# Performance work log

Measured on AMD Instinct MI355X. Metric: run time of the kernel, lower is better.

Reference implementation:

```python
import jax, jax.numpy as jnp
import numpy as np

D_MODEL = 1024
HEADS = 16
D_K = D_MODEL // HEADS
B, S = 2, 2048


def setup_inputs() -> dict:
    key = jax.random.key(0)
    ks = jax.random.split(key, 11)
    sc = 1.0 / np.sqrt(D_MODEL)
    inp = {
        "q": jax.random.normal(ks[0], (B, S, D_MODEL), jnp.float32),
        "k": jax.random.normal(ks[1], (B, S, D_MODEL), jnp.float32),
        "v": jax.random.normal(ks[2], (B, S, D_MODEL), jnp.float32),
        # causal mask, broadcastable to (B, H, S, S); 0 -> masked
        "mask": jnp.tril(jnp.ones((S, S), jnp.int32))[None, None],
        "w_q": jax.random.normal(ks[3], (D_MODEL, D_MODEL), jnp.float32) * sc,
        "b_q": jax.random.normal(ks[4], (D_MODEL,), jnp.float32) * sc,
        "w_k": jax.random.normal(ks[5], (D_MODEL, D_MODEL), jnp.float32) * sc,
        "b_k": jax.random.normal(ks[6], (D_MODEL,), jnp.float32) * sc,
        "w_v": jax.random.normal(ks[7], (D_MODEL, D_MODEL), jnp.float32) * sc,
        "b_v": jax.random.normal(ks[8], (D_MODEL,), jnp.float32) * sc,
        "w_o": jax.random.normal(ks[9], (D_MODEL, D_MODEL), jnp.float32) * sc,
        "b_o": jax.random.normal(ks[10], (D_MODEL,), jnp.float32) * sc,
    }
    return inp


def reference(q, k, v, mask, w_q, b_q, w_k, b_k, w_v, b_v, w_o, b_o):
    b = q.shape[0]
    # torch Linear: x @ W.T + b
    Q = q @ w_q.T + b_q
    K = k @ w_k.T + b_k
    V = v @ w_v.T + b_v
    # (B, S, D) -> (B, H, S, d_k)
    Q = Q.reshape(b, -1, HEADS, D_K).transpose(0, 2, 1, 3)
    K = K.reshape(b, -1, HEADS, D_K).transpose(0, 2, 1, 3)
    V = V.reshape(b, -1, HEADS, D_K).transpose(0, 2, 1, 3)
    scores = jnp.einsum("bhqd,bhkd->bhqk", Q, K) / np.sqrt(D_K).astype(np.float32)
    scores = jnp.where(mask == 0, -jnp.inf, scores)
    attn = jax.nn.softmax(scores, axis=-1)
    out = jnp.einsum("bhqk,bhkd->bhqd", attn, V)
    out = out.transpose(0, 2, 1, 3).reshape(b, -1, D_MODEL)
    # dropout is identity in eval mode
    return out @ w_o.T + b_o
```

## Files before the change

kernel.cpp:

```cpp
#include <hip/hip_runtime.h>
#include <math.h>

#define D_MODEL 1024
#define N_HEADS 16
#define DKH     64
#define BATCH   2
#define SEQ     2048
#define NT128   (SEQ/128)
#define PARTS_PER_BH 40

typedef unsigned short u16;
typedef __attribute__((ext_vector_type(8))) short short8;
typedef __attribute__((ext_vector_type(4))) float f32x4;

__device__ __forceinline__ u16 f2bf(float f) {
    unsigned u = __float_as_uint(f);
    u += 0x7fffu + ((u >> 16) & 1u);
    return (u16)(u >> 16);
}
__device__ __forceinline__ float bf2f(u16 x) {
    return __int_as_float(((int)x) << 16);
}

__device__ __forceinline__ void gll16(const void* g, void* l) {
    __builtin_amdgcn_global_load_lds((const __attribute__((address_space(1))) void*)g,
                                     (__attribute__((address_space(3))) void*)l, 16, 0, 0);
}

template<int CTRL>
__device__ __forceinline__ float rormax(float x) {
    int r = __builtin_amdgcn_update_dpp(__float_as_int(x), __float_as_int(x),
                                        CTRL, 0xf, 0xf, false);
    return fmaxf(x, __int_as_float(r));
}
__device__ __forceinline__ float rowmax16(float x) {
    x = rormax<0x121>(x);
    x = rormax<0x122>(x);
    x = rormax<0x124>(x);
    x = rormax<0x128>(x);
    return x;
}

__global__ __launch_bounds__(256)
void convert_kernel(const float* __restrict__ q, const float* __restrict__ k,
                    const float* __restrict__ v, const float* __restrict__ wq,
                    const float* __restrict__ wk, const float* __restrict__ wv,
                    const float* __restrict__ wo,
                    u16* __restrict__ qb, u16* __restrict__ kb, u16* __restrict__ vb,
                    u16* __restrict__ wqb, u16* __restrict__ wkb,
                    u16* __restrict__ wvb, u16* __restrict__ wob)
{
    const size_t NV = ((size_t)16 << 20) >> 3;
    for (size_t i = (size_t)blockIdx.x * blockDim.x + threadIdx.x; i < NV;
         i += (size_t)gridDim.x * blockDim.x) {
        const size_t e = i << 3;
        const float* s; u16* d; size_t off;
        if (e < ((size_t)12 << 20)) {
            const int seg = (int)(e >> 22);
            off = e & (((size_t)1 << 22) - 1);
            s = seg == 0 ? q : seg == 1 ? k : v;
            d = seg == 0 ? qb : seg == 1 ? kb : vb;
        } else {
            const size_t r = e - ((size_t)12 << 20);
            const int seg = (int)(r >> 20);
            off = r & (((size_t)1 << 20) - 1);
            s = seg == 0 ? wq : seg == 1 ? wk : seg == 2 ? wv : wo;
            d = seg == 0 ? wqb : seg == 1 ? wkb : seg == 2 ? wvb : wob;
        }
        const float4 f0 = *(const float4*)(s + off);
        const float4 f1 = *(const float4*)(s + off + 4);
        short8 o;
        o[0]=(short)f2bf(f0.x); o[1]=(short)f2bf(f0.y); o[2]=(short)f2bf(f0.z); o[3]=(short)f2bf(f0.w);
        o[4]=(short)f2bf(f1.x); o[5]=(short)f2bf(f1.y); o[6]=(short)f2bf(f1.z); o[7]=(short)f2bf(f1.w);
        *(short8*)(d + off) = o;
    }
}

#define GEMM_PREAMBLE                                                            \
    __shared__ __align__(16) u16 As[2][128][32];                                 \
    __shared__ __align__(16) u16 Bs[2][128][32];                                 \
    const int tid  = threadIdx.x;                                                \
    const int lane = tid & 63;                                                   \
    const int wid  = tid >> 6;                                                   \
    const int wm   = wid >> 1, wn = wid & 1;                                     \
    const int lr   = lane & 15, lg = lane >> 4;                                  \
    const int mb   = blockIdx.x * 128, nb = blockIdx.y * 128;                    \
    const int g_row = lane >> 2;                                                 \
    const int g_col = (lane & 3) << 3;                                           \
    const u16* Ab = A  + (size_t)mb * K;                                         \
    const u16* Bb = Bw + (size_t)nb * K;                                         \
    f32x4 acc[4][4];                                                             \
    _Pragma("unroll")                                                            \
    for (int i = 0; i < 4; ++i)                                                  \
        _Pragma("unroll")                                                        \
        for (int j = 0; j < 4; ++j) { f32x4 z = {0.f,0.f,0.f,0.f}; acc[i][j] = z; }

#define STAGE(buf, kt)                                                           \
    {                                                                            \
        _Pragma("unroll")                                                        \
        for (int t = 0; t < 2; ++t) {                                            \
            const int r0 = t*64 + wid*16;                                        \
            gll16(&Ab[(size_t)(r0 + g_row)*K + (kt) + g_col], &As[buf][r0][0]);  \
            gll16(&Bb[(size_t)(r0 + g_row)*K + (kt) + g_col], &Bs[buf][r0][0]);  \
        }                                                                        \
    }

#define GEMM_MAINLOOP                                                            \
    STAGE(0, 0)                                                                  \
    __syncthreads();                                                             \
    const int NK = K >> 5;                                                       \
    for (int it = 0; it < NK; ++it) {                                            \
        const int c = it & 1;                                                    \
        if (it + 1 < NK) STAGE(c ^ 1, (it + 1) << 5)                             \
        short8 a[4], b[4];                                                       \
        _Pragma("unroll")                                                        \
        for (int i = 0; i < 4; ++i) a[i] = *(const short8*)&As[c][wm*64 + i*16 + lr][lg*8]; \
        _Pragma("unroll")                                                        \
        for (int j = 0; j < 4; ++j) b[j] = *(const short8*)&Bs[c][wn*64 + j*16 + lr][lg*8]; \
        _Pragma("unroll")                                                        \
        for (int i = 0; i < 4; ++i)                                              \
            _Pragma("unroll")                                                    \
            for (int j = 0; j < 4; ++j)                                          \
                acc[i][j] = __builtin_amdgcn_mfma_f32_16x16x32_bf16(a[i], b[j], acc[i][j], 0, 0, 0); \
        __syncthreads();                                                         \
    }

__global__ __launch_bounds__(256, 3)
void gemm_qkv_kernel(const u16* __restrict__ qb, const u16* __restrict__ kb,
                     const u16* __restrict__ vb, const u16* __restrict__ wqb,
                     const u16* __restrict__ wkb, const u16* __restrict__ wvb,
                     const float* __restrict__ b_q, const float* __restrict__ b_k,
                     const float* __restrict__ b_v,
                     u16* __restrict__ Qh, u16* __restrict__ Kh, u16* __restrict__ Vt,
                     int M, int N, int K)
{
    const int z = blockIdx.z;
    const u16* A    = z == 0 ? qb  : z == 1 ? kb  : vb;
    const u16* Bw   = z == 0 ? wqb : z == 1 ? wkb : wvb;
    const float* bias = z == 0 ? b_q : z == 1 ? b_k : b_v;
    u16* dst        = z == 0 ? Qh  : z == 1 ? Kh  : Vt;
    const float scale = z == 0 ? 0.125f : 1.0f;

    GEMM_PREAMBLE
    GEMM_MAINLOOP

    #pragma unroll
    for (int i = 0; i < 4; ++i) {
        #pragma unroll
        for (int j = 0; j < 4; ++j) {
            const int mbase = mb + wm*64 + i*16 + lg*4;
            const int n     = nb + wn*64 + j*16 + lr;
            const float bn  = bias[n];
            const int h = n >> 6, d = n & 63;
            #pragma unroll
            for (int r = 0; r < 4; ++r) {
                const int m = mbase + r;
                const int b = m >> 11, s = m & (SEQ - 1);
                const float val = (acc[i][j][r] + bn) * scale;
                if (z == 2)
                    dst[(((size_t)(b*N_HEADS + h))*DKH + d)*SEQ + s] = f2bf(val);
                else
                    dst[(((size_t)(b*N_HEADS + h))*SEQ + s)*DKH + d] = f2bf(val);
            }
        }
    }
}

__global__ __launch_bounds__(256)
void gemm_out_kernel(const u16* __restrict__ A, const u16* __restrict__ Bw,
                     const float* __restrict__ bias, float* __restrict__ dst,
                     int M, int N, int K)
{
    GEMM_PREAMBLE
    GEMM_MAINLOOP

    #pragma unroll
    for (int i = 0; i < 4; ++i) {
        #pragma unroll
        for (int j = 0; j < 4; ++j) {
            const int mbase = mb + wm*64 + i*16 + lg*4;
            const int n     = nb + wn*64 + j*16 + lr;
            const float bn  = bias[n];
            #pragma unroll
            for (int r = 0; r < 4; ++r)
                dst[(size_t)(mbase + r) * N + n] = acc[i][j][r] + bn;
        }
    }
}

__device__ __forceinline__ void attn_step(
    const short8& aq0, const short8& aq1,
    f32x4 (&o)[4], f32x4& osum, float (&m_run)[4],
    const u16 (*__restrict__ Kl)[64], const u16 (*__restrict__ Vl)[64],
    u16 (*__restrict__ Pw)[72],
    int kvb, int qbw, int lr, int lg)
{
    const int ksw = (lr & 7) << 3;
    f32x4 s[4];
    #pragma unroll
    for (int cb = 0; cb < 4; ++cb) {
        const int kr = cb*16 + lr;
        f32x4 z = {0.f,0.f,0.f,0.f};
        short8 k0 = *(const short8*)&Kl[kr][( 0 + lg*8) ^ ksw];
        short8 k1 = *(const short8*)&Kl[kr][(32 + lg*8) ^ ksw];
        z = __builtin_amdgcn_mfma_f32_16x16x32_bf16(aq0, k0, z, 0, 0, 0);
        z = __builtin_amdgcn_mfma_f32_16x16x32_bf16(aq1, k1, z, 0, 0, 0);
        s[cb] = z;
    }

    if (kvb + 63 > qbw) {
        #pragma unroll
        for (int cb = 0; cb < 4; ++cb)
            #pragma unroll
            for (int r = 0; r < 4; ++r)
                if (kvb + cb*16 + lr > qbw + lg*4 + r) s[cb][r] = -INFINITY;
    }

    float tm[4];
    #pragma unroll
    for (int r = 0; r < 4; ++r)
        tm[r] = rowmax16(fmaxf(fmaxf(s[0][r], s[1][r]), fmaxf(s[2][r], s[3][r])));

    int need = 0;
    #pragma unroll
    for (int r = 0; r < 4; ++r) need |= (tm[r] > m_run[r] + 8.f) ? 1 : 0;
    if (__any(need)) {
        #pragma unroll
        for (int r = 0; r < 4; ++r) {
            const float mnew  = fmaxf(m_run[r], tm[r]);
            const float alpha = __expf(m_run[r] - mnew);
            m_run[r] = mnew;
            osum[r] *= alpha;
            #pragma unroll
            for (int db = 0; db < 4; ++db) o[db][r] *= alpha;
        }
    }
    #pragma unroll
    for (int r = 0; r < 4; ++r)
        #pragma unroll
        for (int cb = 0; cb < 4; ++cb)
            Pw[lg*4 + r][cb*16 + lr] = f2bf(__expf(s[cb][r] - m_run[r]));

    short8 vone;
    #pragma unroll
    for (int j = 0; j < 8; ++j) vone[j] = (short)0x3F80;
    #pragma unroll
    for (int ks = 0; ks < 2; ++ks) {
        short8 ap = *(short8*)&Pw[lr][ks*32 + lg*8];
        #pragma unroll
        for (int db = 0; db < 4; ++db) {
            const int vr = db*16 + lr;
            short8 bv = *(const short8*)&Vl[vr][(ks*32 + lg*8) ^ ksw];
            o[db] = __builtin_amdgcn_mfma_f32_16x16x32_bf16(ap, bv, o[db], 0, 0, 0);
        }
        osum = __builtin_amdgcn_mfma_f32_16x16x32_bf16(ap, vone, osum, 0, 0, 0);
    }
}

__global__ __launch_bounds__(512)
void flash_split_kernel(const u16* __restrict__ Qh, const u16* __restrict__ Kh,
                        const u16* __restrict__ Vt, u16* __restrict__ part_o,
                        float* __restrict__ part_ms)
{
    __shared__ __align__(16) u16 Kl[2][64][64];
    __shared__ __align__(16) u16 Vl[2][64][64];
    __shared__ __align__(16) u16 P[8][16][72];

    const int x = blockIdx.x;
    int t, ch;
    if      (x <  4) { t = x;                 ch = 0;        }
    else if (x < 12) { t = 4 + ((x-4) >> 1);  ch = (x-4)&1;  }
    else if (x < 24) { t = 8 + (x-12)/3;      ch = (x-12)%3; }
    else             { t = 12 + ((x-24) >> 2); ch = (x-24)&3; }

    const int tid  = threadIdx.x;
    const int lane = tid & 63;
    const int wid  = tid >> 6;
    const int lr   = lane & 15, lg = lane >> 4;
    const int bh   = blockIdx.y;
    const int qbw  = t*128 + wid*16;
    const size_t base = (size_t)bh * SEQ * DKH;

    const int c0      = ch * 8;
    const int nc_here = min(8, 2*(t+1) - c0);

    const int srow = tid >> 3;
    const int se0  = (tid & 7) << 3;
    const int sec  = se0 ^ ((srow & 7) << 3);

    short8 aq0 = *(const short8*)&Qh[base + (size_t)(qbw + lr)*DKH +  0 + lg*8];
    short8 aq1 = *(const short8*)&Qh[base + (size_t)(qbw + lr)*DKH + 32 + lg*8];

    f32x4 o[4], osum;
    float m_run[4];
    #pragma unroll
    for (int r = 0; r < 4; ++r) m_run[r] = -INFINITY;
    {
        f32x4 z = {0.f,0.f,0.f,0.f};
        osum = z;
        #pragma unroll
        for (int db = 0; db < 4; ++db) o[db] = z;
    }

    {
        const int kb0 = c0 * 64;
        short8 k0 = *(const short8*)&Kh[base + (size_t)(kb0 + srow)*DKH + se0];
        short8 v0 = *(const short8*)&Vt[base + (size_t)srow*SEQ + kb0 + se0];
        *(short8*)&Kl[0][srow][sec] = k0;
        *(short8*)&Vl[0][srow][sec] = v0;
    }
    __syncthreads();

    int cur = 0;
    for (int ci = 0; ci < nc_here; ++ci) {
        const int kvb = (c0 + ci) * 64;
        short8 nk0, nv0;
        const bool pref = (ci + 1 < nc_here);
        if (pref) {
            const int nb_ = kvb + 64;
            nk0 = *(const short8*)&Kh[base + (size_t)(nb_ + srow)*DKH + se0];
            nv0 = *(const short8*)&Vt[base + (size_t)srow*SEQ + nb_ + se0];
        }

        if (kvb <= qbw + 15)
            attn_step(aq0, aq1, o, osum, m_run, Kl[cur], Vl[cur], P[wid], kvb, qbw, lr, lg);

        __syncthreads();
        if (pref) {
            *(short8*)&Kl[cur^1][srow][sec] = nk0;
            *(short8*)&Vl[cur^1][srow][sec] = nv0;
        }
        __syncthreads();
        cur ^= 1;
    }

    const size_t slot = (size_t)bh * PARTS_PER_BH + x;
    u16*   po = part_o  + (slot << 13);
    float* pm = part_ms + (slot << 8);
    #pragma unroll
    for (int db = 0; db < 4; ++db)
        #pragma unroll
        for (int r = 0; r < 4; ++r)
            po[(wid*16 + lg*4 + r)*64 + db*16 + lr] = f2bf(o[db][r]);
    if (lr == 0) {
        #pragma unroll
        for (int r = 0; r < 4; ++r) {
            pm[(wid*16 + lg*4 + r)*2 + 0] = m_run[r];
            pm[(wid*16 + lg*4 + r)*2 + 1] = osum[r];
        }
    }
}

__global__ __launch_bounds__(256)
void merge_kernel(const u16* __restrict__ part_o, const float* __restrict__ part_ms,
                  u16* __restrict__ attb)
{
    const int t   = blockIdx.x;
    const int bh  = blockIdx.y;
    const int nch = min(4, (2*(t+1) + 7) >> 3);
    const int basex = t < 4 ? t : t < 8 ? 4 + 2*(t-4) : t < 12 ? 12 + 3*(t-8) : 24 + 4*(t-12);

    const int row = threadIdx.x >> 1;
    const int cb  = (threadIdx.x & 1) * 32;

    float mm[4], ss[4];
    float M = -INFINITY;
    for (int c = 0; c < nch; ++c) {
        const size_t slot = (size_t)bh * PARTS_PER_BH + basex + c;
        mm[c] = part_ms[(slot << 8) + row*2 + 0];
        ss[c] = part_ms[(slot << 8) + row*2 + 1];
        M = fmaxf(M, mm[c]);
    }
    float S = 0.f;
    float acc[32];
    #pragma unroll
    for (int j = 0; j < 32; ++j) acc[j] = 0.f;
    for (int c = 0; c < nch; ++c) {
        const float w = __expf(mm[c] - M);
        S += w * ss[c];
        const size_t slot = (size_t)bh * PARTS_PER_BH + basex + c;
        const u16* po = part_o + (slot << 13) + row*64 + cb;
        #pragma unroll
        for (int g = 0; g < 4; ++g) {
            short8 v = *(const short8*)(po + g*8);
            #pragma unroll
            for (int j = 0; j < 8; ++j)
                acc[g*8 + j] += w * bf2f((u16)v[j]);
        }
    }
    const float inv = 1.f / S;
    const int b = bh >> 4, h = bh & 15;
    const int grow = t*128 + row;
    u16* dst = attb + ((size_t)(b*SEQ + grow))*D_MODEL + h*64 + cb;
    #pragma unroll
    for (int g = 0; g < 4; ++g) {
        short8 ov;
        #pragma unroll
        for (int j = 0; j < 8; ++j) ov[j] = (short)f2bf(acc[g*8 + j] * inv);
        *(short8*)(dst + g*8) = ov;
    }
}

extern "C" void kernel_launch(void* const* d_in, const int* in_sizes, int n_in,
                              void* d_out, int out_size, void* d_ws, size_t ws_size,
                              hipStream_t stream)
{
    const float* q   = (const float*)d_in[0];
    const float* k   = (const float*)d_in[1];
    const float* v   = (const float*)d_in[2];
    const float* w_q = (const float*)d_in[4];
    const float* b_q = (const float*)d_in[5];
    const float* w_k = (const float*)d_in[6];
    const float* b_k = (const float*)d_in[7];
    const float* w_v = (const float*)d_in[8];
    const float* b_v = (const float*)d_in[9];
    const float* w_o = (const float*)d_in[10];
    const float* b_o = (const float*)d_in[11];

    char* ws = (char*)d_ws;
    const size_t MB = 1024*1024;
    u16* Qh   = (u16*)(ws +  0*MB);
    u16* Kh   = (u16*)(ws +  8*MB);
    u16* Vt   = (u16*)(ws + 16*MB);
    u16* qb   = (u16*)(ws + 24*MB);
    u16* kb   = (u16*)(ws + 32*MB);
    u16* vb   = (u16*)(ws + 40*MB);
    u16* wqb  = (u16*)(ws + 48*MB);
    u16* wkb  = (u16*)(ws + 50*MB);
    u16* wvb  = (u16*)(ws + 52*MB);
    u16* wob  = (u16*)(ws + 54*MB);
    u16* attb = qb;
    u16*   part_o  = (u16*)(ws + 32*MB);
    float* part_ms = (float*)(ws + 52*MB);

    const int M = BATCH * SEQ, N = D_MODEL, K = D_MODEL;

    convert_kernel<<<2048, 256, 0, stream>>>(q, k, v, w_q, w_k, w_v, w_o,
                                             qb, kb, vb, wqb, wkb, wvb, wob);
    gemm_qkv_kernel<<<dim3(M/128, N/128, 3), 256, 0, stream>>>(
        qb, kb, vb, wqb, wkb, wvb, b_q, b_k, b_v, Qh, Kh, Vt, M, N, K);
    flash_split_kernel<<<dim3(PARTS_PER_BH, BATCH*N_HEADS), 512, 0, stream>>>(
        Qh, Kh, Vt, part_o, part_ms);
    merge_kernel<<<dim3(NT128, BATCH*N_HEADS), 256, 0, stream>>>(part_o, part_ms, attb);
    gemm_out_kernel<<<dim3(M/128, N/128), 256, 0, stream>>>(attb, wob, b_o, (float*)d_out, M, N, K);
}
```

Before: 143.6 us.

## Shrink out-projection GEMM tile, single-buffer flash KV, add MFMA priority hints

The output-projection GEMM moves from 128x128 to 128x64 tiles with its own inline main loop, doubling the grid to fill more CUs. The flash kernel drops its double-buffered K/V shared memory in favour of a single buffer, adds an occupancy hint to launch bounds, and wraps its MFMA sections in s_setprio. The aim is more concurrent blocks and waves per CU, with MFMA issue favoured over other work. The trade-off is less reuse per GEMM block and less room for copy/compute overlap in the flash loop, although the existing two syncs already make the single buffer safe.

```diff
diff --git a/kernel.cpp b/kernel.cpp
--- a/kernel.cpp
+++ b/kernel.cpp
@@ -171,15 +171,66 @@
                      const float* __restrict__ bias, float* __restrict__ dst,
                      int M, int N, int K)
 {
-    GEMM_PREAMBLE
-    GEMM_MAINLOOP
+    __shared__ __align__(16) u16 As[2][128][32];
+    __shared__ __align__(16) u16 Bs[2][64][32];
+
+    const int tid  = threadIdx.x;
+    const int lane = tid & 63;
+    const int wid  = tid >> 6;
+    const int wm   = wid >> 1, wn = wid & 1;
+    const int lr   = lane & 15, lg = lane >> 4;
+    const int mb   = blockIdx.x * 128, nb = blockIdx.y * 64;
+    const int g_row = lane >> 2;
+    const int g_col = (lane & 3) << 3;
+
+    const u16* Ab = A  + (size_t)mb * K;
+    const u16* Bb = Bw + (size_t)nb * K;
+
+    f32x4 acc[4][2];
+    #pragma unroll
+    for (int i = 0; i < 4; ++i)
+        #pragma unroll
+        for (int j = 0; j < 2; ++j) { f32x4 z = {0.f,0.f,0.f,0.f}; acc[i][j] = z; }
+
+#define OSTAGE(buf, kt)                                                          \
+    {                                                                            \
+        _Pragma("unroll")                                                        \
+        for (int t = 0; t < 2; ++t) {                                            \
+            const int r0 = t*64 + wid*16;                                        \
+            gll16(&Ab[(size_t)(r0 + g_row)*K + (kt) + g_col], &As[buf][r0][0]);  \
+        }                                                                        \
+        gll16(&Bb[(size_t)(wid*16 + g_row)*K + (kt) + g_col], &Bs[buf][wid*16][0]); \
+    }
+
+    OSTAGE(0, 0)
+    __syncthreads();
+
+    const int NK = K >> 5;
+    for (int it = 0; it < NK; ++it) {
+        const int c = it & 1;
+        if (it + 1 < NK) OSTAGE(c ^ 1, (it + 1) << 5)
+
+        short8 a[4], b[2];
+        #pragma unroll
+        for (int i = 0; i < 4; ++i) a[i] = *(const short8*)&As[c][wm*64 + i*16 + lr][lg*8];
+        #pragma unroll
+        for (int j = 0; j < 2; ++j) b[j] = *(const short8*)&Bs[c][wn*32 + j*16 + lr][lg*8];
+        #pragma unroll
+        for (int i = 0; i < 4; ++i)
+            #pragma unroll
+            for (int j = 0; j < 2; ++j)
+                acc[i][j] = __builtin_amdgcn_mfma_f32_16x16x32_bf16(a[i], b[j], acc[i][j], 0, 0, 0);
+
+        __syncthreads();
+    }
+#undef OSTAGE
 
     #pragma unroll
     for (int i = 0; i < 4; ++i) {
         #pragma unroll
-        for (int j = 0; j < 4; ++j) {
+        for (int j = 0; j < 2; ++j) {
             const int mbase = mb + wm*64 + i*16 + lg*4;
-            const int n     = nb + wn*64 + j*16 + lr;
+            const int n     = nb + wn*32 + j*16 + lr;
             const float bn  = bias[n];
             #pragma unroll
             for (int r = 0; r < 4; ++r)
@@ -197,6 +248,7 @@
 {
     const int ksw = (lr & 7) << 3;
     f32x4 s[4];
+    __builtin_amdgcn_s_setprio(1);
     #pragma unroll
     for (int cb = 0; cb < 4; ++cb) {
         const int kr = cb*16 + lr;
@@ -207,6 +259,7 @@
         z = __builtin_amdgcn_mfma_f32_16x16x32_bf16(aq1, k1, z, 0, 0, 0);
         s[cb] = z;
     }
+    __builtin_amdgcn_s_setprio(0);
 
     if (kvb + 63 > qbw) {
         #pragma unroll
@@ -244,6 +297,7 @@
     short8 vone;
     #pragma unroll
     for (int j = 0; j < 8; ++j) vone[j] = (short)0x3F80;
+    __builtin_amdgcn_s_setprio(1);
     #pragma unroll
     for (int ks = 0; ks < 2; ++ks) {
         short8 ap = *(short8*)&Pw[lr][ks*32 + lg*8];
@@ -255,15 +309,16 @@
         }
         osum = __builtin_amdgcn_mfma_f32_16x16x32_bf16(ap, vone, osum, 0, 0, 0);
     }
-}
-
-__global__ __launch_bounds__(512)
+    __builtin_amdgcn_s_setprio(0);
+}
+
+__global__ __launch_bounds__(512, 8)
 void flash_split_kernel(const u16* __restrict__ Qh, const u16* __restrict__ Kh,
                         const u16* __restrict__ Vt, u16* __restrict__ part_o,
                         float* __restrict__ part_ms)
 {
-    __shared__ __align__(16) u16 Kl[2][64][64];
-    __shared__ __align__(16) u16 Vl[2][64][64];
+    __shared__ __align__(16) u16 Kl[64][64];
+    __shared__ __align__(16) u16 Vl[64][64];
     __shared__ __align__(16) u16 P[8][16][72];
 
     const int x = blockIdx.x;
@@ -306,12 +361,11 @@
         const int kb0 = c0 * 64;
         short8 k0 = *(const short8*)&Kh[base + (size_t)(kb0 + srow)*DKH + se0];
         short8 v0 = *(const short8*)&Vt[base + (size_t)srow*SEQ + kb0 + se0];
-        *(short8*)&Kl[0][srow][sec] = k0;
-        *(short8*)&Vl[0][srow][sec] = v0;
+        *(short8*)&Kl[srow][sec] = k0;
+        *(short8*)&Vl[srow][sec] = v0;
     }
     __syncthreads();
 
-    int cur = 0;
     for (int ci = 0; ci < nc_here; ++ci) {
         const int kvb = (c0 + ci) * 64;
         short8 nk0, nv0;
@@ -323,15 +377,14 @@
         }
 
         if (kvb <= qbw + 15)
-            attn_step(aq0, aq1, o, osum, m_run, Kl[cur], Vl[cur], P[wid], kvb, qbw, lr, lg);
+            attn_step(aq0, aq1, o, osum, m_run, Kl, Vl, P[wid], kvb, qbw, lr, lg);
 
         __syncthreads();
         if (pref) {
-            *(short8*)&Kl[cur^1][srow][sec] = nk0;
-            *(short8*)&Vl[cur^1][srow][sec] = nv0;
+            *(short8*)&Kl[srow][sec] = nk0;
+            *(short8*)&Vl[srow][sec] = nv0;
         }
         __syncthreads();
-        cur ^= 1;
     }
 
     const size_t slot = (size_t)bh * PARTS_PER_BH + x;
@@ -442,5 +495,5 @@
     flash_split_kernel<<<dim3(PARTS_PER_BH, BATCH*N_HEADS), 512, 0, stream>>>(
         Qh, Kh, Vt, part_o, part_ms);
     merge_kernel<<<dim3(NT128, BATCH*N_HEADS), 256, 0, stream>>>(part_o, part_ms, attb);
-    gemm_out_kernel<<<dim3(M/128, N/128), 256, 0, stream>>>(attb, wob, b_o, (float*)d_out, M, N, K);
-}
+    gemm_out_kernel<<<dim3(M/128, N/64), 256, 0, stream>>>(attb, wob, b_o, (float*)d_out, M, N, K);
+}
```

Result: slower. 170.6 us (+18.8%).
